# Performance work log

Measured on AMD Instinct MI355X. Metric: run time of the kernel, lower is better.

Reference implementation:

```python
import math
import jax, jax.numpy as jnp
import numpy as np

B, T, D, H = 4, 1024, 1024, 8
HD = D // H  # head_dim = 128

def _trigram_dirs():
    # 8 trigrams = all sign combinations in {−1,+1}^3, L2-normalized (p=2, dim=1)
    t = np.array([[(i >> b & 1) * 2 - 1 for b in (2, 1, 0)] for i in range(8)], dtype=np.float32)
    return jnp.asarray(t / np.linalg.norm(t, axis=1, keepdims=True))

def setup_inputs() -> dict:
    key = jax.random.key(0)
    k1, k2, k3, k4 = jax.random.split(key, 4)
    x = jax.random.normal(k1, (B, T, D), dtype=jnp.float32)
    Wqkv = jax.random.normal(k2, (D, 3 * D), dtype=jnp.float32) * 0.02
    Wout = jax.random.normal(k3, (D, D), dtype=jnp.float32) * 0.02
    # head_scales init to 0 in the module; use nonzero values so the geo-bias path is exercised
    head_scales = jax.random.normal(k4, (H,), dtype=jnp.float32) * 0.1
    head_dirs = _trigram_dirs()  # [H, 3] buffer
    return {"x": x, "Wqkv": Wqkv, "Wout": Wout, "head_scales": head_scales, "head_dirs": head_dirs}

def reference(x, Wqkv, Wout, head_scales, head_dirs):
    b, t, d = x.shape
    scale = 1.0 / math.sqrt(HD)
    qkv = (x @ Wqkv).reshape(b, t, 3, H, HD)
    qkv = jnp.transpose(qkv, (2, 0, 3, 1, 4))  # [3, B, H, T, HD]
    q, k, v = qkv[0], qkv[1], qkv[2]
    # scores: [B, H, T, T]
    scores = jnp.einsum('bhqd,bhkd->bhqk', q, k) * scale
    # rank-1 trigram geometric bias from first 3 dims of q/k
    q_proj = jnp.einsum('bhtd,hd->bht', q[..., :3], head_dirs)
    k_proj = jnp.einsum('bhtd,hd->bht', k[..., :3], head_dirs)
    geo_bias = q_proj[..., :, None] * k_proj[..., None, :]  # [B, H, T, T]
    scores = scores + head_scales[None, :, None, None] * geo_bias
    causal = jnp.tril(jnp.ones((t, t), dtype=bool))
    scores = jnp.where(causal, scores, -jnp.inf)
    attn = jax.nn.softmax(scores, axis=-1)
    out = jnp.einsum('bhqk,bhkd->bhqd', attn, v)  # [B, H, T, HD]
    out = jnp.transpose(out, (0, 2, 1, 3)).reshape(b, t, d)
    return out @ Wout
```

## Files before the change

### kernel.cpp

```cpp
#include <hip/hip_runtime.h>
#include <stdint.h>

typedef __attribute__((ext_vector_type(8))) short short8;
typedef __attribute__((ext_vector_type(4))) short short4v;
typedef __attribute__((ext_vector_type(4))) float f32x4;

__device__ __forceinline__ short f2bf(float x) {
  union { float f; uint32_t u; } c; c.f = x;
  uint32_t r = (c.u + 0x7FFFu + ((c.u >> 16) & 1u)) >> 16;
  return (short)r;
}
__device__ __forceinline__ float b2f(short s) {
  union { uint32_t u; float f; } c; c.u = ((uint32_t)(uint16_t)s) << 16;
  return c.f;
}
__device__ __forceinline__ uint32_t pack2bf(float lo, float hi) {
  return ((uint32_t)(uint16_t)f2bf(hi) << 16) | (uint32_t)(uint16_t)f2bf(lo);
}

__global__ __launch_bounds__(256) void cvt_kernel(const float* __restrict__ in,
                                                  short* __restrict__ out, int n4) {
  int i = blockIdx.x * 256 + threadIdx.x;
  const int stride = gridDim.x * 256;
  for (; i < n4; i += stride) {
    float4 v = reinterpret_cast<const float4*>(in)[i];
    short4v o;
    o.x = f2bf(v.x); o.y = f2bf(v.y); o.z = f2bf(v.z); o.w = f2bf(v.w);
    reinterpret_cast<short4v*>(out)[i] = o;
  }
}

__global__ __launch_bounds__(256) void tcvt_kernel(const float* __restrict__ in,
                                                   short* __restrict__ out, int K, int N) {
  __shared__ __align__(16) short tile[32][33];
  const int nb = blockIdx.x * 32, kb = blockIdx.y * 32;
  const int tx = threadIdx.x & 31, ty = threadIdx.x >> 5;
#pragma unroll
  for (int i = 0; i < 32; i += 8)
    tile[ty + i][tx] = f2bf(in[(size_t)(kb + ty + i) * N + nb + tx]);
  __syncthreads();
#pragma unroll
  for (int i = 0; i < 32; i += 8)
    out[(size_t)(nb + ty + i) * K + kb + tx] = tile[tx][ty + i];
}

__global__ __launch_bounds__(256) void vtrans_kernel(const short* __restrict__ qkvb,
                                                     short* __restrict__ vT) {
  __shared__ __align__(16) short tile[64][65];
  const int b = blockIdx.z;
  const int kv0 = blockIdx.x * 64, c0 = blockIdx.y * 64;
  const int tx = threadIdx.x & 15, ty = threadIdx.x >> 4;
  const short* src = qkvb + (size_t)(b * 1024) * 3072 + 2048;
#pragma unroll
  for (int i = 0; i < 64; i += 16) {
    int r = ty + i;
#pragma unroll
    for (int j = 0; j < 4; ++j)
      tile[r][tx * 4 + j] = src[(size_t)(kv0 + r) * 3072 + c0 + tx * 4 + j];
  }
  __syncthreads();
  short* dst = vT + (size_t)b * 1024 * 1024;
#pragma unroll
  for (int i = 0; i < 64; i += 16) {
    int cc = ty + i;
#pragma unroll
    for (int j = 0; j < 4; ++j)
      dst[(size_t)(c0 + cc) * 1024 + kv0 + tx * 4 + j] = tile[tx * 4 + j][cc];
  }
}

__global__ __launch_bounds__(256) void kproj_kernel(const short* __restrict__ qkvb,
                                                    const float* __restrict__ hdirs,
                                                    float* __restrict__ kproj) {
  const int i = blockIdx.x * 256 + threadIdx.x;
  const int bh = i >> 10, tt = i & 1023;
  const int b = bh >> 3, h = bh & 7;
  const float d0 = hdirs[h * 3], d1 = hdirs[h * 3 + 1], d2 = hdirs[h * 3 + 2];
  const short* kr = qkvb + (size_t)(b * 1024 + tt) * 3072 + 1024 + h * 128;
  kproj[i] = b2f(kr[0]) * d0 + b2f(kr[1]) * d1 + b2f(kr[2]) * d2;
}

template <int OUT_BF16>
__global__ __launch_bounds__(256) void gemm_kernel(const short* __restrict__ A,
                                                   const short* __restrict__ Bt,
                                                   void* __restrict__ Cout,
                                                   int K, int ldc) {
  __shared__ __align__(16) short Al[2][128 * 32];
  __shared__ __align__(16) short Bl[2][128 * 32];
  const int t = threadIdx.x;
  const int lane = t & 63, w = t >> 6;
  const int wr = w >> 1, wc = w & 1;
  const int g = lane >> 4, c16 = lane & 15;
  const int row0 = blockIdx.y * 128, col0 = blockIdx.x * 128;

  f32x4 acc[4][4];
#pragma unroll
  for (int m = 0; m < 4; ++m)
#pragma unroll
    for (int n = 0; n < 4; ++n) {
      f32x4 z = {0.0f, 0.0f, 0.0f, 0.0f};
      acc[m][n] = z;
    }

  auto stage = [&](int buf, int kt) {
    const int k0 = kt * 32;
#pragma unroll
    for (int i = 0; i < 2; ++i) {
      const int qb = i * 256 + (t & 192);
      const int q = qb + lane;
      const int r = q >> 2;
      const int c = (q & 3) ^ ((r >> 1) & 3);
      const short* ga = A + (size_t)(row0 + r) * K + k0 + c * 8;
      const short* gb = Bt + (size_t)(col0 + r) * K + k0 + c * 8;
      __builtin_amdgcn_global_load_lds((const __attribute__((address_space(1))) void*)ga,
                                       (__attribute__((address_space(3))) void*)&Al[buf][qb * 8],
                                       16, 0, 0);
      __builtin_amdgcn_global_load_lds((const __attribute__((address_space(1))) void*)gb,
                                       (__attribute__((address_space(3))) void*)&Bl[buf][qb * 8],
                                       16, 0, 0);
    }
  };

  stage(0, 0);
  __syncthreads();
  const int NK = K >> 5;
  int cur = 0;
  const int rA0 = wr * 64 + c16;
  const int rB0 = wc * 64 + c16;
  for (int kt = 0; kt < NK; ++kt) {
    if (kt + 1 < NK) stage(cur ^ 1, kt + 1);
    short8 aF[4], bF[4];
#pragma unroll
    for (int m = 0; m < 4; ++m) {
      const int r = rA0 + m * 16;
      const int c = g ^ ((r >> 1) & 3);
      aF[m] = *reinterpret_cast<const short8*>(&Al[cur][r * 32 + c * 8]);
    }
#pragma unroll
    for (int n = 0; n < 4; ++n) {
      const int r = rB0 + n * 16;
      const int c = g ^ ((r >> 1) & 3);
      bF[n] = *reinterpret_cast<const short8*>(&Bl[cur][r * 32 + c * 8]);
    }
#pragma unroll
    for (int m = 0; m < 4; ++m)
#pragma unroll
      for (int n = 0; n < 4; ++n)
        acc[m][n] = __builtin_amdgcn_mfma_f32_16x16x32_bf16(aF[m], bF[n], acc[m][n], 0, 0, 0);
    __syncthreads();
    cur ^= 1;
  }

  const int er = row0 + wr * 64 + g * 4;
  const int ec = col0 + wc * 64 + c16;
#pragma unroll
  for (int m = 0; m < 4; ++m)
#pragma unroll
    for (int n = 0; n < 4; ++n)
#pragma unroll
      for (int j = 0; j < 4; ++j) {
        const size_t off = (size_t)(er + m * 16 + j) * ldc + ec + n * 16;
        if (OUT_BF16)
          ((short*)Cout)[off] = f2bf(acc[m][n][j]);
        else
          ((float*)Cout)[off] = acc[m][n][j];
      }
}

__global__ __launch_bounds__(256) void attn_kernel(const short* __restrict__ qkvb,
                                                   const short* __restrict__ vT,
                                                   const float* __restrict__ head_scales,
                                                   const float* __restrict__ hdirs,
                                                   const float* __restrict__ kproj,
                                                   short* __restrict__ attnb) {
  __shared__ __align__(16) short Kl[2][64 * 128];
  __shared__ __align__(16) short Vl[2][128 * 64];
  __shared__ float kp_lds[2][64];

  const int bid = blockIdx.x;
  const int bh = (bid & 7) * 4 + ((bid >> 3) & 3);
  const int qt = 15 - (bid >> 5);
  const int b = bh >> 3, h = bh & 7;
  const int t = threadIdx.x, lane = t & 63, w = t >> 6;
  const int g = lane >> 4, c16 = lane & 15;
  const int q0w = qt * 64 + w * 16;
  const int q_abs = q0w + c16;

  const short* qbase = qkvb + (size_t)(b * 1024) * 3072 + h * 128;
  const short* kbase = qbase + 1024;
  const short* vtb = vT + (size_t)bh * 128 * 1024;
  const float* kp = kproj + bh * 1024;

  const float LOG2E = 1.44269504088896f;
  const float scale2 = 0.08838834764831845f * 1.44269504088896f;

  short8 aQ[4];
  float hqp;
  {
    const short* qr = qbase + (size_t)(q0w + c16) * 3072;
#pragma unroll
    for (int kk = 0; kk < 4; ++kk)
      aQ[kk] = *reinterpret_cast<const short8*>(qr + kk * 32 + g * 8);
    const float hs = head_scales[h];
    hqp = hs * LOG2E *
          (b2f(qr[0]) * hdirs[h * 3] + b2f(qr[1]) * hdirs[h * 3 + 1] + b2f(qr[2]) * hdirs[h * 3 + 2]);
  }

  float m_s = -1e30f, l_s = 0.0f;
  f32x4 accO[8];
#pragma unroll
  for (int d = 0; d < 8; ++d) {
    f32x4 z = {0.0f, 0.0f, 0.0f, 0.0f};
    accO[d] = z;
  }

  auto stageKV = [&](int buf, int kvt) {
    const int kv0 = kvt * 64;
#pragma unroll
    for (int i = 0; i < 4; ++i) {
      const int s = w * 4 + i;
      {
        const int r = s * 4 + g;
        const int c = c16 ^ (r & 7);
        const short* ga = kbase + (size_t)(kv0 + r) * 3072 + c * 8;
        __builtin_amdgcn_global_load_lds((const __attribute__((address_space(1))) void*)ga,
                                         (__attribute__((address_space(3))) void*)&Kl[buf][s * 512],
                                         16, 0, 0);
      }
      {
        const int r = s * 8 + (lane >> 3);
        const int c = (lane & 7) ^ (r & 7);
        const short* ga = vtb + (size_t)r * 1024 + kv0 + c * 8;
        __builtin_amdgcn_global_load_lds((const __attribute__((address_space(1))) void*)ga,
                                         (__attribute__((address_space(3))) void*)&Vl[buf][s * 512],
                                         16, 0, 0);
      }
    }
    if (lane < 16) kp_lds[buf][w * 16 + lane] = kp[kv0 + w * 16 + lane];
  };

  const int nkv = qt + 1;
  stageKV(0, 0);
  __syncthreads();
  int cur = 0;
  for (int kvt = 0; kvt < nkv; ++kvt) {
    const int kv0 = kvt * 64;
    if (kvt + 1 < nkv) stageKV(cur ^ 1, kvt + 1);
    const short* Kc = Kl[cur];
    const short* Vc = Vl[cur];
    const float* kpc = kp_lds[cur];

    float p[4][4];
#pragma unroll
    for (int n = 0; n < 4; ++n) {
      f32x4 s4 = {0.0f, 0.0f, 0.0f, 0.0f};
      const int r = n * 16 + c16;
#pragma unroll
      for (int kk = 0; kk < 4; ++kk) {
        const int cch = (kk * 4 + g) ^ (r & 7);
        short8 bK = *reinterpret_cast<const short8*>(&Kc[r * 128 + cch * 8]);
        s4 = __builtin_amdgcn_mfma_f32_16x16x32_bf16(bK, aQ[kk], s4, 0, 0, 0);
      }
#pragma unroll
      for (int j = 0; j < 4; ++j) {
        const int kloc = n * 16 + g * 4 + j;
        const float v = s4[j] * scale2 + hqp * kpc[kloc];
        p[n][j] = (kv0 + kloc <= q_abs) ? v : -1e30f;
      }
    }

    float mx;
    {
      float a0 = fmaxf(fmaxf(p[0][0], p[0][1]), fmaxf(p[0][2], p[0][3]));
      float a1 = fmaxf(fmaxf(p[1][0], p[1][1]), fmaxf(p[1][2], p[1][3]));
      float a2 = fmaxf(fmaxf(p[2][0], p[2][1]), fmaxf(p[2][2], p[2][3]));
      float a3 = fmaxf(fmaxf(p[3][0], p[3][1]), fmaxf(p[3][2], p[3][3]));
      mx = fmaxf(fmaxf(a0, a1), fmaxf(a2, a3));
      mx = fmaxf(mx, __shfl_xor(mx, 16, 64));
      mx = fmaxf(mx, __shfl_xor(mx, 32, 64));
    }

    if (__any(mx - m_s > 11.54f)) {
      const float mn = fmaxf(m_s, mx);
      const float alpha = exp2f(m_s - mn);
      m_s = mn;
      l_s *= alpha;
      float aO[4];
#pragma unroll
      for (int j = 0; j < 4; ++j) aO[j] = __shfl(alpha, g * 4 + j, 64);
#pragma unroll
      for (int d = 0; d < 8; ++d)
#pragma unroll
        for (int j = 0; j < 4; ++j) accO[d][j] *= aO[j];
    }

    float s01 = 0.0f, s23 = 0.0f;
#pragma unroll
    for (int n = 0; n < 4; ++n) {
      float e0 = exp2f(p[n][0] - m_s), e1 = exp2f(p[n][1] - m_s);
      float e2 = exp2f(p[n][2] - m_s), e3 = exp2f(p[n][3] - m_s);
      p[n][0] = e0; p[n][1] = e1; p[n][2] = e2; p[n][3] = e3;
      if (n < 2) s01 += (e0 + e1) + (e2 + e3); else s23 += (e0 + e1) + (e2 + e3);
    }
    float sum = s01 + s23;
    sum += __shfl_xor(sum, 16, 64);
    sum += __shfl_xor(sum, 32, 64);
    l_s += sum;

    uint32_t pk[4][2];
#pragma unroll
    for (int n = 0; n < 4; ++n) {
      pk[n][0] = pack2bf(p[n][0], p[n][1]);
      pk[n][1] = pack2bf(p[n][2], p[n][3]);
    }

    union { uint32_t d[4]; short8 s; } aPu[2];
#pragma unroll
    for (int kk = 0; kk < 2; ++kk)
#pragma unroll
      for (int wd = 0; wd < 4; ++wd) {
        const int src = (2 * (g & 1) + (wd >> 1)) * 16 + c16;
        const uint32_t v0 = (uint32_t)__shfl((int)pk[kk * 2][wd & 1], src, 64);
        const uint32_t v1 = (uint32_t)__shfl((int)pk[kk * 2 + 1][wd & 1], src, 64);
        aPu[kk].d[wd] = (g >= 2) ? v1 : v0;
      }

#pragma unroll
    for (int dt = 0; dt < 8; ++dt) {
      const int r = dt * 16 + c16;
#pragma unroll
      for (int kk = 0; kk < 2; ++kk) {
        const int cch = (kk * 4 + g) ^ (r & 7);
        short8 bV = *reinterpret_cast<const short8*>(&Vc[r * 64 + cch * 8]);
        accO[dt] = __builtin_amdgcn_mfma_f32_16x16x32_bf16(aPu[kk].s, bV, accO[dt], 0, 0, 0);
      }
    }
    __syncthreads();
    cur ^= 1;
  }

  float linv[4];
#pragma unroll
  for (int j = 0; j < 4; ++j) linv[j] = 1.0f / __shfl(l_s, g * 4 + j, 64);
#pragma unroll
  for (int j = 0; j < 4; ++j) {
    const size_t rowoff = (size_t)(b * 1024 + q0w + g * 4 + j) * 1024 + h * 128;
#pragma unroll
    for (int dt = 0; dt < 8; ++dt)
      attnb[rowoff + dt * 16 + c16] = f2bf(accO[dt][j] * linv[j]);
  }
}

extern "C" void kernel_launch(void* const* d_in, const int* in_sizes, int n_in,
                              void* d_out, int out_size, void* d_ws, size_t ws_size,
                              hipStream_t stream) {
  const float* x = (const float*)d_in[0];
  const float* Wqkv = (const float*)d_in[1];
  const float* Wout = (const float*)d_in[2];
  const float* hscale = (const float*)d_in[3];
  const float* hdirs = (const float*)d_in[4];
  float* out = (float*)d_out;

  char* ws = (char*)d_ws;
  short* xb = (short*)(ws);
  short* wqkvT = (short*)(ws + (size_t)8 * 1024 * 1024);
  short* woutT = (short*)(ws + (size_t)14 * 1024 * 1024);
  short* qkvb = (short*)(ws + (size_t)16 * 1024 * 1024);
  short* vT = (short*)(ws + (size_t)40 * 1024 * 1024);
  short* attnb = (short*)(ws + (size_t)48 * 1024 * 1024);
  float* kproj = (float*)(ws);

  cvt_kernel<<<2048, 256, 0, stream>>>(x, xb, (4 * 1024 * 1024) / 4);
  tcvt_kernel<<<dim3(96, 32), 256, 0, stream>>>(Wqkv, wqkvT, 1024, 3072);
  tcvt_kernel<<<dim3(32, 32), 256, 0, stream>>>(Wout, woutT, 1024, 1024);
  gemm_kernel<1><<<dim3(24, 32), 256, 0, stream>>>(xb, wqkvT, (void*)qkvb, 1024, 3072);
  kproj_kernel<<<128, 256, 0, stream>>>(qkvb, hdirs, kproj);
  vtrans_kernel<<<dim3(16, 16, 4), 256, 0, stream>>>(qkvb, vT);
  attn_kernel<<<512, 256, 0, stream>>>(qkvb, vT, hscale, hdirs, kproj, attnb);
  gemm_kernel<0><<<dim3(8, 32), 256, 0, stream>>>(attnb, woutT, out, 1024, 1024);
}
```

Measured before the change: 120.6 us.

## Replace QKV projection GEMM with 256x256-tile kernel using direct global-to-LDS loads

Adds a new 512-thread GEMM kernel for the QKV projection. It uses 256x256 output tiles with K-step 64, async global_load_lds staging into double-buffered, XOR-swizzled LDS, and a quarter-by-quarter MFMA schedule that interleaves loads and compute. Workgroup indices are remapped so neighbouring tiles land on the same XCD, and MFMA sections get raised wave priority. The aim is higher arithmetic intensity and better load/compute overlap than the 128x128 kernel. The trade-off is a grid of only 192 blocks with large LDS use, which may leave some CUs idle.

After: 125.7 us. 4.2% more time.

```diff
diff --git a/kernel.cpp b/kernel.cpp
--- a/kernel.cpp
+++ b/kernel.cpp
@@ -78,6 +78,146 @@
   const float d0 = hdirs[h * 3], d1 = hdirs[h * 3 + 1], d2 = hdirs[h * 3 + 2];
   const short* kr = qkvb + (size_t)(b * 1024 + tt) * 3072 + 1024 + h * 128;
   kproj[i] = b2f(kr[0]) * d0 + b2f(kr[1]) * d1 + b2f(kr[2]) * d2;
+}
+
+__device__ __forceinline__ void stage_half256(const short* __restrict__ gsrc,
+                                              int K, short* lds_half,
+                                              int w, int lane) {
+#pragma unroll
+  for (int i = 0; i < 2; ++i) {
+    const int chunk = w * 2 + i;
+    const int rr = chunk * 8 + (lane >> 3);
+    const int cc = ((lane & 7) * 8) ^ (((rr >> 2) & 1) << 4);
+    const short* ga = gsrc + (size_t)rr * K + cc;
+    __builtin_amdgcn_global_load_lds((const __attribute__((address_space(1))) void*)ga,
+                                     (__attribute__((address_space(3))) void*)(lds_half + chunk * 512),
+                                     16, 0, 0);
+  }
+}
+
+template <int OUT_BF16>
+__global__ __launch_bounds__(512, 2) void gemm256_kernel(const short* __restrict__ A,
+                                                         const short* __restrict__ Bt,
+                                                         void* __restrict__ Cout,
+                                                         int K, int ldc, int nbx) {
+  __shared__ __align__(16) short Al[2][256 * 64];
+  __shared__ __align__(16) short Bl[2][256 * 64];
+  const int t = threadIdx.x;
+  const int lane = t & 63, w = t >> 6;
+  const int wr = w >> 2, wc = w & 3;
+  const int g = lane >> 4, c16 = lane & 15;
+  const int nwg = gridDim.x;
+  const int swz = (blockIdx.x & 7) * (nwg >> 3) + (blockIdx.x >> 3);
+  const int row0 = (swz / nbx) * 256, col0 = (swz % nbx) * 256;
+
+  f32x4 acc[8][4];
+#pragma unroll
+  for (int m = 0; m < 8; ++m)
+#pragma unroll
+    for (int n = 0; n < 4; ++n) {
+      f32x4 z = {0.0f, 0.0f, 0.0f, 0.0f};
+      acc[m][n] = z;
+    }
+
+  const int NT = K >> 6;
+#define STAGE_A(H, KT, BUF) stage_half256(A + (size_t)(row0 + (H)*128) * K + (KT)*64, K, &Al[BUF][(H)*8192], w, lane)
+#define STAGE_B(H, KT, BUF) stage_half256(Bt + (size_t)(col0 + (H)*128) * K + (KT)*64, K, &Bl[BUF][(H)*8192], w, lane)
+
+  STAGE_A(0, 0, 0); STAGE_B(0, 0, 0); STAGE_A(1, 0, 0); STAGE_B(1, 0, 0);
+  if (NT > 1) {
+    STAGE_A(0, 1, 1); STAGE_B(0, 1, 1);
+    asm volatile("s_waitcnt vmcnt(4)");
+  } else {
+    asm volatile("s_waitcnt vmcnt(0)");
+  }
+  __builtin_amdgcn_s_barrier();
+
+  short8 aF[4][2], bFa[2][2], bFb[2][2];
+
+#define LDA(MG, BUF)                                                                   \
+  {                                                                                    \
+    _Pragma("unroll") for (int mi = 0; mi < 4; ++mi) {                                 \
+      const int r = (MG)*128 + wr * 64 + mi * 16 + c16;                                \
+      const int sx = ((r >> 2) & 1) << 4;                                              \
+      aF[mi][0] = *reinterpret_cast<const short8*>(&Al[BUF][r * 64 + ((g * 8) ^ sx)]); \
+      aF[mi][1] = *reinterpret_cast<const short8*>(&Al[BUF][r * 64 + ((32 + g * 8) ^ sx)]); \
+    }                                                                                  \
+  }
+#define LDB(NG, DST, BUF)                                                              \
+  {                                                                                    \
+    _Pragma("unroll") for (int ni = 0; ni < 2; ++ni) {                                 \
+      const int r = (NG)*128 + wc * 32 + ni * 16 + c16;                                \
+      const int sx = ((r >> 2) & 1) << 4;                                              \
+      DST[ni][0] = *reinterpret_cast<const short8*>(&Bl[BUF][r * 64 + ((g * 8) ^ sx)]); \
+      DST[ni][1] = *reinterpret_cast<const short8*>(&Bl[BUF][r * 64 + ((32 + g * 8) ^ sx)]); \
+    }                                                                                  \
+  }
+#define DOMFMA(MG, NG, BF)                                                             \
+  __builtin_amdgcn_s_setprio(1);                                                       \
+  _Pragma("unroll") for (int mi = 0; mi < 4; ++mi) {                                   \
+    _Pragma("unroll") for (int ni = 0; ni < 2; ++ni) {                                 \
+      acc[(MG)*4 + mi][(NG)*2 + ni] = __builtin_amdgcn_mfma_f32_16x16x32_bf16(         \
+          aF[mi][0], BF[ni][0], acc[(MG)*4 + mi][(NG)*2 + ni], 0, 0, 0);               \
+      acc[(MG)*4 + mi][(NG)*2 + ni] = __builtin_amdgcn_mfma_f32_16x16x32_bf16(         \
+          aF[mi][1], BF[ni][1], acc[(MG)*4 + mi][(NG)*2 + ni], 0, 0, 0);               \
+    }                                                                                  \
+  }                                                                                    \
+  __builtin_amdgcn_s_setprio(0);
+
+  for (int kt = 0; kt < NT; ++kt) {
+    const int buf = kt & 1;
+    LDA(0, buf);
+    LDB(0, bFa, buf);
+    if (kt + 1 < NT) STAGE_A(1, kt + 1, buf ^ 1);
+    __builtin_amdgcn_s_barrier();
+    asm volatile("s_waitcnt lgkmcnt(0)");
+    DOMFMA(0, 0, bFa);
+    __builtin_amdgcn_s_barrier();
+    LDB(1, bFb, buf);
+    if (kt + 1 < NT) STAGE_B(1, kt + 1, buf ^ 1);
+    __builtin_amdgcn_s_barrier();
+    asm volatile("s_waitcnt lgkmcnt(0)");
+    DOMFMA(0, 1, bFb);
+    __builtin_amdgcn_s_barrier();
+    LDA(1, buf);
+    if (kt + 2 < NT) STAGE_A(0, kt + 2, buf);
+    __builtin_amdgcn_s_barrier();
+    asm volatile("s_waitcnt lgkmcnt(0)");
+    DOMFMA(1, 0, bFa);
+    __builtin_amdgcn_s_barrier();
+    if (kt + 2 < NT) STAGE_B(0, kt + 2, buf);
+    if (kt == NT - 2) {
+      asm volatile("s_waitcnt vmcnt(0)");
+    } else if (kt < NT - 2) {
+      asm volatile("s_waitcnt vmcnt(4)");
+    }
+    __builtin_amdgcn_s_barrier();
+    asm volatile("s_waitcnt lgkmcnt(0)");
+    DOMFMA(1, 1, bFb);
+    __builtin_amdgcn_s_barrier();
+  }
+#undef LDA
+#undef LDB
+#undef DOMFMA
+#undef STAGE_A
+#undef STAGE_B
+
+#pragma unroll
+  for (int mf = 0; mf < 8; ++mf) {
+    const int er = row0 + (mf >> 2) * 128 + wr * 64 + (mf & 3) * 16 + g * 4;
+#pragma unroll
+    for (int nf = 0; nf < 4; ++nf) {
+      const int ec = col0 + (nf >> 1) * 128 + wc * 32 + (nf & 1) * 16 + c16;
+#pragma unroll
+      for (int j = 0; j < 4; ++j) {
+        const size_t off = (size_t)(er + j) * ldc + ec;
+        if (OUT_BF16)
+          ((short*)Cout)[off] = f2bf(acc[mf][nf][j]);
+        else
+          ((float*)Cout)[off] = acc[mf][nf][j];
+      }
+    }
+  }
 }
 
 template <int OUT_BF16>
@@ -373,7 +513,7 @@
   cvt_kernel<<<2048, 256, 0, stream>>>(x, xb, (4 * 1024 * 1024) / 4);
   tcvt_kernel<<<dim3(96, 32), 256, 0, stream>>>(Wqkv, wqkvT, 1024, 3072);
   tcvt_kernel<<<dim3(32, 32), 256, 0, stream>>>(Wout, woutT, 1024, 1024);
-  gemm_kernel<1><<<dim3(24, 32), 256, 0, stream>>>(xb, wqkvT, (void*)qkvb, 1024, 3072);
+  gemm256_kernel<1><<<192, 512, 0, stream>>>(xb, wqkvT, (void*)qkvb, 1024, 3072, 12);
   kproj_kernel<<<128, 256, 0, stream>>>(qkvb, hdirs, kproj);
   vtrans_kernel<<<dim3(16, 16, 4), 256, 0, stream>>>(qkvb, vT);
   attn_kernel<<<512, 256, 0, stream>>>(qkvb, vT, hscale, hdirs, kproj, attnb);
```
